# Optimization experiments

Hardware: AMD Instinct MI355X
Metric: run time of the kernel (lower is better)

The kernel has to match this reference:

```python
import math
import jax, jax.numpy as jnp
import numpy as np

B, T, IN_DIM = 8, 2048, 256
HEAD_TOTAL = 256  # out_dim * n_heads
NEG = -1e9


def make_mask(t):
    # torch: tril(ones, diagonal=-1).bool() -> masked_fill(-1e9)
    # i.e., entry (i, j) is -1e9 when j < i (anti-causal), 0 otherwise.
    i = jnp.arange(t)[:, None]
    j = jnp.arange(t)[None, :]
    return jnp.where(j < i, jnp.float32(NEG), jnp.float32(0.0))  # [T, T]


def setup_inputs() -> dict:
    key = jax.random.key(0)
    kx, kq, kk = jax.random.split(key, 3)
    x = jax.random.normal(kx, (B, T, IN_DIM), dtype=jnp.float32)
    # nn.Linear weights are [out_features, in_features]
    s = 1.0 / math.sqrt(IN_DIM)
    Wq = jax.random.uniform(kq, (HEAD_TOTAL, IN_DIM), dtype=jnp.float32, minval=-s, maxval=s)
    Wk = jax.random.uniform(kk, (HEAD_TOTAL, IN_DIM), dtype=jnp.float32, minval=-s, maxval=s)
    return {"x": x, "Wq": Wq, "Wk": Wk}


def reference(x, Wq, Wk):
    # q, k: [B, T, HEAD_TOTAL]
    q = jnp.einsum('bti,oi->bto', x, Wq)
    k = jnp.einsum('bsi,oi->bso', x, Wk)
    scale = 1.0 / math.sqrt(x.shape[-1])  # sqrt(in_dim), as in the source
    mask = make_mask(x.shape[1])
    # e: [B, T, T] masked pre-softmax scores (what the torch forward computes)
    e = jnp.einsum('bto,bso->bts', q, k) * scale + mask
    return e
```

## Files before the change

### kernel.cpp

```cpp
#include <hip/hip_runtime.h>
#include <hip/hip_bf16.h>
#include <stdint.h>

#define B_DIM 8
#define T_DIM 2048
#define INNER 256
#define NEGV (-1e9f)
#define SCALE 0.0625f

typedef __bf16 bf16_t;
typedef __bf16 bf16x8 __attribute__((ext_vector_type(8)));
typedef float f32x4 __attribute__((ext_vector_type(4)));

__device__ inline void gload_lds16(const bf16_t* g, bf16_t* lds) {
  __builtin_amdgcn_global_load_lds(
      (__attribute__((address_space(1))) void*)(g),
      (__attribute__((address_space(3))) void*)(lds),
      16, 0, 0);
}

__device__ inline void stage_tile(const bf16_t* gbase, int ldg,
                                  bf16_t (*lds)[64], int tid) {
  const int l = tid & 63;
  const int w = tid >> 6;
  const int sub = l >> 3;
  const int ce = (l & 7) * 8;
#pragma unroll
  for (int i = 0; i < 4; ++i) {
    const int chunk = i * 4 + w;
    const int row = chunk * 8 + sub;
    gload_lds16(gbase + (size_t)row * ldg + ce, &lds[chunk * 8][0]);
  }
}

__device__ inline void stage_tile_cvt(const float* gbase, int ldg,
                                      bf16_t (*lds)[64], int tid) {
  const int l = tid & 63;
  const int w = tid >> 6;
  const int sub = l >> 3;
  const int ce = (l & 7) * 8;
  f32x4 v[4][2];
#pragma unroll
  for (int i = 0; i < 4; ++i) {
    const int row = (i * 4 + w) * 8 + sub;
    const float* p = gbase + (size_t)row * ldg + ce;
    v[i][0] = *(const f32x4*)p;
    v[i][1] = *(const f32x4*)(p + 4);
  }
#pragma unroll
  for (int i = 0; i < 4; ++i) {
    const int row = (i * 4 + w) * 8 + sub;
    bf16x8 o;
#pragma unroll
    for (int j = 0; j < 4; ++j) {
      o[j]     = (bf16_t)v[i][0][j];
      o[4 + j] = (bf16_t)v[i][1][j];
    }
    *(bf16x8*)&lds[row][ce] = o;
  }
}

template <int KDIM>
__device__ inline void gemm_bt_128(const bf16_t* A, const bf16_t* Bm, int ld,
                                   bf16_t (*Al)[64], bf16_t (*Bl)[64],
                                   f32x4 acc[4][4], int tid) {
  const int l = tid & 63;
  const int wid = tid >> 6;
  const int wr = wid >> 1, wc = wid & 1;
  const int lr = l & 15;
  const int kg = l >> 4;
#pragma unroll
  for (int k0 = 0; k0 < KDIM; k0 += 64) {
    stage_tile(A + k0, ld, Al, tid);
    stage_tile(Bm + k0, ld, Bl, tid);
    __syncthreads();
#pragma unroll
    for (int kk = 0; kk < 2; ++kk) {
      bf16x8 af[4], bfm[4];
#pragma unroll
      for (int f = 0; f < 4; ++f) {
        af[f]  = *(const bf16x8*)&Al[wr * 64 + f * 16 + lr][kk * 32 + kg * 8];
        bfm[f] = *(const bf16x8*)&Bl[wc * 64 + f * 16 + lr][kk * 32 + kg * 8];
      }
#pragma unroll
      for (int m = 0; m < 4; ++m)
#pragma unroll
        for (int n = 0; n < 4; ++n)
          acc[m][n] = __builtin_amdgcn_mfma_f32_16x16x32_bf16(
              af[m], bfm[n], acc[m][n], 0, 0, 0);
    }
    __syncthreads();
  }
}

__global__ __launch_bounds__(256) void proj_kernel(
    const float* __restrict__ x, const float* __restrict__ Wq,
    const float* __restrict__ Wk, bf16_t* __restrict__ Q,
    bf16_t* __restrict__ Kout) {
  __shared__ bf16_t Al[128][64];
  __shared__ bf16_t Bl[128][64];
  const int tid = threadIdx.x;
  const int mrow = blockIdx.x * 128;
  const int ncol = blockIdx.y * 128;
  const float* W = blockIdx.z ? Wk : Wq;
  bf16_t* O = blockIdx.z ? Kout : Q;

  const int l = tid & 63, wid = tid >> 6, wr = wid >> 1, wc = wid & 1;
  const int lr = l & 15, kg = l >> 4;

  f32x4 acc[4][4] = {};
  const float* Ax = x + (size_t)mrow * INNER;
  const float* Bw = W + (size_t)ncol * INNER;
#pragma unroll
  for (int k0 = 0; k0 < INNER; k0 += 64) {
    stage_tile_cvt(Ax + k0, INNER, Al, tid);
    stage_tile_cvt(Bw + k0, INNER, Bl, tid);
    __syncthreads();
#pragma unroll
    for (int kk = 0; kk < 2; ++kk) {
      bf16x8 af[4], bfm[4];
#pragma unroll
      for (int f = 0; f < 4; ++f) {
        af[f]  = *(const bf16x8*)&Al[wr * 64 + f * 16 + lr][kk * 32 + kg * 8];
        bfm[f] = *(const bf16x8*)&Bl[wc * 64 + f * 16 + lr][kk * 32 + kg * 8];
      }
#pragma unroll
      for (int m = 0; m < 4; ++m)
#pragma unroll
        for (int n = 0; n < 4; ++n)
          acc[m][n] = __builtin_amdgcn_mfma_f32_16x16x32_bf16(
              af[m], bfm[n], acc[m][n], 0, 0, 0);
    }
    __syncthreads();
  }

#pragma unroll
  for (int m = 0; m < 4; ++m)
#pragma unroll
    for (int n = 0; n < 4; ++n)
#pragma unroll
      for (int j = 0; j < 4; ++j) {
        int r = mrow + wr * 64 + m * 16 + kg * 4 + j;
        int c = ncol + wc * 64 + n * 16 + lr;
        O[(size_t)r * INNER + c] = (bf16_t)acc[m][n][j];
      }
}

__global__ __launch_bounds__(256) void scores_kernel(
    const bf16_t* __restrict__ Q, const bf16_t* __restrict__ Kin,
    float* __restrict__ E) {
  const int bid = blockIdx.x;
  const int b = bid & 7;
  const int lid = bid >> 3;
  const int rt = lid >> 4;
  const int ct = lid & 15;
  const int tid = threadIdx.x;
  float* Eb = E + (size_t)b * T_DIM * T_DIM;
  const int trow = rt * 128, scol = ct * 128;

  if (ct < rt) {
    const f32x4 neg = {NEGV, NEGV, NEGV, NEGV};
#pragma unroll
    for (int it = 0; it < 16; ++it) {
      int idx = it * 256 + tid;
      int r = idx >> 5, c4 = idx & 31;
      *(f32x4*)&Eb[(size_t)(trow + r) * T_DIM + scol + c4 * 4] = neg;
    }
    return;
  }

  __shared__ bf16_t Al[128][64];
  __shared__ bf16_t Bl[128][64];
  f32x4 acc[4][4] = {};
  const bf16_t* Qb = Q + (size_t)b * T_DIM * INNER;
  const bf16_t* Kb = Kin + (size_t)b * T_DIM * INNER;
  gemm_bt_128<INNER>(Qb + (size_t)trow * INNER, Kb + (size_t)scol * INNER,
                     INNER, Al, Bl, acc, tid);

  const int l = tid & 63, wid = tid >> 6, wr = wid >> 1, wc = wid & 1;
  const int lr = l & 15, kg = l >> 4;
  const bool diag = (ct == rt);
#pragma unroll
  for (int m = 0; m < 4; ++m)
#pragma unroll
    for (int n = 0; n < 4; ++n)
#pragma unroll
      for (int j = 0; j < 4; ++j) {
        int t = trow + wr * 64 + m * 16 + kg * 4 + j;
        int s = scol + wc * 64 + n * 16 + lr;
        float v = acc[m][n][j] * SCALE;
        if (diag && s < t) v += NEGV;
        Eb[(size_t)t * T_DIM + s] = v;
      }
}

extern "C" void kernel_launch(void* const* d_in, const int* in_sizes, int n_in,
                              void* d_out, int out_size, void* d_ws,
                              size_t ws_size, hipStream_t stream) {
  const float* x  = (const float*)d_in[0];
  const float* Wq = (const float*)d_in[1];
  const float* Wk = (const float*)d_in[2];
  float* out = (float*)d_out;

  const size_t n_x = (size_t)B_DIM * T_DIM * INNER;

  bf16_t* Q = (bf16_t*)d_ws;
  bf16_t* K = Q + n_x;

  dim3 g1(B_DIM * T_DIM / 128, INNER / 128, 2);
  proj_kernel<<<g1, dim3(256), 0, stream>>>(x, Wq, Wk, Q, K);

  scores_kernel<<<2048, 256, 0, stream>>>(Q, K, out);
}
```

Before: 47.08 us.

## Widen score tiles to 128x256 with 512-thread blocks

The scores kernel now uses 128x256 output tiles computed by 8 waves instead of 128x128 tiles with 4 waves, halving the block count. Each staged Q tile is reused across twice as many key columns, which cuts redundant global-to-LDS traffic. The fill-only blocks for the fully masked region and the diagonal mask test are adjusted to the wider tiles. The cost is coarser granularity along the diagonal: some tiles that straddle it compute scores that end up masked, and each block uses more LDS.

```diff
diff --git a/kernel.cpp b/kernel.cpp
--- a/kernel.cpp
+++ b/kernel.cpp
@@ -19,15 +19,16 @@
       16, 0, 0);
 }
 
-__device__ inline void stage_tile(const bf16_t* gbase, int ldg,
-                                  bf16_t (*lds)[64], int tid) {
+template <int ROWS>
+__device__ inline void stage_tile512(const bf16_t* gbase, int ldg,
+                                     bf16_t (*lds)[64], int tid) {
   const int l = tid & 63;
   const int w = tid >> 6;
   const int sub = l >> 3;
   const int ce = (l & 7) * 8;
 #pragma unroll
-  for (int i = 0; i < 4; ++i) {
-    const int chunk = i * 4 + w;
+  for (int i = 0; i < ROWS / 64; ++i) {
+    const int chunk = i * 8 + w;
     const int row = chunk * 8 + sub;
     gload_lds16(gbase + (size_t)row * ldg + ce, &lds[chunk * 8][0]);
   }
@@ -57,39 +58,6 @@
       o[4 + j] = (bf16_t)v[i][1][j];
     }
     *(bf16x8*)&lds[row][ce] = o;
-  }
-}
-
-template <int KDIM>
-__device__ inline void gemm_bt_128(const bf16_t* A, const bf16_t* Bm, int ld,
-                                   bf16_t (*Al)[64], bf16_t (*Bl)[64],
-                                   f32x4 acc[4][4], int tid) {
-  const int l = tid & 63;
-  const int wid = tid >> 6;
-  const int wr = wid >> 1, wc = wid & 1;
-  const int lr = l & 15;
-  const int kg = l >> 4;
-#pragma unroll
-  for (int k0 = 0; k0 < KDIM; k0 += 64) {
-    stage_tile(A + k0, ld, Al, tid);
-    stage_tile(Bm + k0, ld, Bl, tid);
-    __syncthreads();
-#pragma unroll
-    for (int kk = 0; kk < 2; ++kk) {
-      bf16x8 af[4], bfm[4];
-#pragma unroll
-      for (int f = 0; f < 4; ++f) {
-        af[f]  = *(const bf16x8*)&Al[wr * 64 + f * 16 + lr][kk * 32 + kg * 8];
-        bfm[f] = *(const bf16x8*)&Bl[wc * 64 + f * 16 + lr][kk * 32 + kg * 8];
-      }
-#pragma unroll
-      for (int m = 0; m < 4; ++m)
-#pragma unroll
-        for (int n = 0; n < 4; ++n)
-          acc[m][n] = __builtin_amdgcn_mfma_f32_16x16x32_bf16(
-              af[m], bfm[n], acc[m][n], 0, 0, 0);
-    }
-    __syncthreads();
   }
 }
 
@@ -146,40 +114,63 @@
       }
 }
 
-__global__ __launch_bounds__(256) void scores_kernel(
+__global__ __launch_bounds__(512) void scores_kernel(
     const bf16_t* __restrict__ Q, const bf16_t* __restrict__ Kin,
     float* __restrict__ E) {
   const int bid = blockIdx.x;
   const int b = bid & 7;
   const int lid = bid >> 3;
-  const int rt = lid >> 4;
-  const int ct = lid & 15;
+  const int rt = lid >> 3;
+  const int ct = lid & 7;
   const int tid = threadIdx.x;
   float* Eb = E + (size_t)b * T_DIM * T_DIM;
-  const int trow = rt * 128, scol = ct * 128;
-
-  if (ct < rt) {
+  const int trow = rt * 128, scol = ct * 256;
+
+  if (scol + 256 <= trow) {
     const f32x4 neg = {NEGV, NEGV, NEGV, NEGV};
 #pragma unroll
     for (int it = 0; it < 16; ++it) {
-      int idx = it * 256 + tid;
-      int r = idx >> 5, c4 = idx & 31;
+      int idx = it * 512 + tid;
+      int r = idx >> 6, c4 = idx & 63;
       *(f32x4*)&Eb[(size_t)(trow + r) * T_DIM + scol + c4 * 4] = neg;
     }
     return;
   }
 
   __shared__ bf16_t Al[128][64];
-  __shared__ bf16_t Bl[128][64];
+  __shared__ bf16_t Bl[256][64];
+  const int l = tid & 63;
+  const int w = tid >> 6;
+  const int wr = w >> 2, wc = w & 3;
+  const int lr = l & 15, kg = l >> 4;
+
   f32x4 acc[4][4] = {};
-  const bf16_t* Qb = Q + (size_t)b * T_DIM * INNER;
-  const bf16_t* Kb = Kin + (size_t)b * T_DIM * INNER;
-  gemm_bt_128<INNER>(Qb + (size_t)trow * INNER, Kb + (size_t)scol * INNER,
-                     INNER, Al, Bl, acc, tid);
-
-  const int l = tid & 63, wid = tid >> 6, wr = wid >> 1, wc = wid & 1;
-  const int lr = l & 15, kg = l >> 4;
-  const bool diag = (ct == rt);
+  const bf16_t* Qb = Q + ((size_t)b * T_DIM + trow) * INNER;
+  const bf16_t* Kb = Kin + ((size_t)b * T_DIM + scol) * INNER;
+#pragma unroll
+  for (int k0 = 0; k0 < INNER; k0 += 64) {
+    stage_tile512<128>(Qb + k0, INNER, Al, tid);
+    stage_tile512<256>(Kb + k0, INNER, Bl, tid);
+    __syncthreads();
+#pragma unroll
+    for (int kk = 0; kk < 2; ++kk) {
+      bf16x8 af[4], bfm[4];
+#pragma unroll
+      for (int f = 0; f < 4; ++f) {
+        af[f]  = *(const bf16x8*)&Al[wr * 64 + f * 16 + lr][kk * 32 + kg * 8];
+        bfm[f] = *(const bf16x8*)&Bl[wc * 64 + f * 16 + lr][kk * 32 + kg * 8];
+      }
+#pragma unroll
+      for (int m = 0; m < 4; ++m)
+#pragma unroll
+        for (int n = 0; n < 4; ++n)
+          acc[m][n] = __builtin_amdgcn_mfma_f32_16x16x32_bf16(
+              af[m], bfm[n], acc[m][n], 0, 0, 0);
+    }
+    __syncthreads();
+  }
+
+  const bool maskable = (scol < trow + 128);
 #pragma unroll
   for (int m = 0; m < 4; ++m)
 #pragma unroll
@@ -189,7 +180,7 @@
         int t = trow + wr * 64 + m * 16 + kg * 4 + j;
         int s = scol + wc * 64 + n * 16 + lr;
         float v = acc[m][n][j] * SCALE;
-        if (diag && s < t) v += NEGV;
+        if (maskable && s < t) v += NEGV;
         Eb[(size_t)t * T_DIM + s] = v;
       }
 }
@@ -210,5 +201,5 @@
   dim3 g1(B_DIM * T_DIM / 128, INNER / 128, 2);
   proj_kernel<<<g1, dim3(256), 0, stream>>>(x, Wq, Wk, Q, K);
 
-  scores_kernel<<<2048, 256, 0, stream>>>(Q, K, out);
-}
+  scores_kernel<<<1024, 512, 0, stream>>>(Q, K, out);
+}
```

Measured after the change: 56.32 us. 19.6% more time.

## Move masked-tile fill into projection kernel to overlap with projection GEMM

Applied to the files above, without the earlier changes.

The -1e9 fill of strictly lower-triangular score tiles moves out of the scores kernel and into the projection kernel. Fill blocks are interleaved with projection compute blocks (odd block ids compute, the rest fill), and a triangular index is recovered with a sqrt formula. The point is to overlap the write-bound fill with the compute-bound projection and to shorten the scores kernel. The costs are a bigger first launch and the reliance on float sqrt to decode the tile index, which the code corrects with a fixup.

```diff
diff --git a/kernel.cpp b/kernel.cpp
--- a/kernel.cpp
+++ b/kernel.cpp
@@ -1,6 +1,7 @@
 #include <hip/hip_runtime.h>
 #include <hip/hip_bf16.h>
 #include <stdint.h>
+#include <math.h>
 
 #define B_DIM 8
 #define T_DIM 2048
@@ -93,18 +94,43 @@
   }
 }
 
-__global__ __launch_bounds__(256) void proj_kernel(
+__global__ __launch_bounds__(256) void proj_fill_kernel(
     const float* __restrict__ x, const float* __restrict__ Wq,
     const float* __restrict__ Wk, bf16_t* __restrict__ Q,
-    bf16_t* __restrict__ Kout) {
+    bf16_t* __restrict__ Kout, float* __restrict__ E) {
+  const int bid = blockIdx.x;
+  const int tid = threadIdx.x;
+
+  const bool is_compute = (bid < 1024) && (bid & 1);
+  if (!is_compute) {
+    int fidx = (bid < 1024) ? (bid >> 1) : (bid - 512);
+    const int b = fidx / 120;
+    int r = fidx - b * 120;
+    int rt = (int)((1.0f + sqrtf(1.0f + 8.0f * (float)r)) * 0.5f);
+    int ct = r - ((rt * (rt - 1)) >> 1);
+    if (ct >= rt) { ct -= rt; rt += 1; }
+    else if (ct < 0) { rt -= 1; ct = r - ((rt * (rt - 1)) >> 1); }
+    float* Eb = E + (size_t)b * T_DIM * T_DIM;
+    const int trow = rt * 128, scol = ct * 128;
+    const f32x4 neg = {NEGV, NEGV, NEGV, NEGV};
+#pragma unroll
+    for (int it = 0; it < 16; ++it) {
+      int idx = it * 256 + tid;
+      int rr = idx >> 5, c4 = idx & 31;
+      *(f32x4*)&Eb[(size_t)(trow + rr) * T_DIM + scol + c4 * 4] = neg;
+    }
+    return;
+  }
+
+  const int idx = bid >> 1;
+  const int mrow = (idx & 127) * 128;
+  const int ncol = ((idx >> 7) & 1) * 128;
+  const int z = idx >> 8;
+  const float* W = z ? Wk : Wq;
+  bf16_t* O = z ? Kout : Q;
+
   __shared__ bf16_t Al[128][64];
   __shared__ bf16_t Bl[128][64];
-  const int tid = threadIdx.x;
-  const int mrow = blockIdx.x * 128;
-  const int ncol = blockIdx.y * 128;
-  const float* W = blockIdx.z ? Wk : Wq;
-  bf16_t* O = blockIdx.z ? Kout : Q;
-
   const int l = tid & 63, wid = tid >> 6, wr = wid >> 1, wc = wid & 1;
   const int lr = l & 15, kg = l >> 4;
 
@@ -140,9 +166,9 @@
     for (int n = 0; n < 4; ++n)
 #pragma unroll
       for (int j = 0; j < 4; ++j) {
-        int r = mrow + wr * 64 + m * 16 + kg * 4 + j;
-        int c = ncol + wc * 64 + n * 16 + lr;
-        O[(size_t)r * INNER + c] = (bf16_t)acc[m][n][j];
+        int rr = mrow + wr * 64 + m * 16 + kg * 4 + j;
+        int cc = ncol + wc * 64 + n * 16 + lr;
+        O[(size_t)rr * INNER + cc] = (bf16_t)acc[m][n][j];
       }
 }
 
@@ -154,20 +180,10 @@
   const int lid = bid >> 3;
   const int rt = lid >> 4;
   const int ct = lid & 15;
+  if (ct < rt) return;
   const int tid = threadIdx.x;
   float* Eb = E + (size_t)b * T_DIM * T_DIM;
   const int trow = rt * 128, scol = ct * 128;
-
-  if (ct < rt) {
-    const f32x4 neg = {NEGV, NEGV, NEGV, NEGV};
-#pragma unroll
-    for (int it = 0; it < 16; ++it) {
-      int idx = it * 256 + tid;
-      int r = idx >> 5, c4 = idx & 31;
-      *(f32x4*)&Eb[(size_t)(trow + r) * T_DIM + scol + c4 * 4] = neg;
-    }
-    return;
-  }
 
   __shared__ bf16_t Al[128][64];
   __shared__ bf16_t Bl[128][64];
@@ -207,8 +223,7 @@
   bf16_t* Q = (bf16_t*)d_ws;
   bf16_t* K = Q + n_x;
 
-  dim3 g1(B_DIM * T_DIM / 128, INNER / 128, 2);
-  proj_kernel<<<g1, dim3(256), 0, stream>>>(x, Wq, Wk, Q, K);
+  proj_fill_kernel<<<1472, 256, 0, stream>>>(x, Wq, Wk, Q, K, out);
 
   scores_kernel<<<2048, 256, 0, stream>>>(Q, K, out);
 }
```

Measured after the change: 53.76 us. 1.14x slower.

## Load MFMA operands directly from global memory in scores kernel, drop LDS staging

Applied to the files above, without the earlier changes.

The scores kernel no longer stages Q and K tiles into shared memory with global_load_lds and barriers. Each lane now reads its bf16x8 MFMA fragments straight from global memory, relying on L1/L2 to serve the overlapping reads across waves. This removes the LDS traffic and __syncthreads, at the cost of duplicated global loads across the 2x2 wave grid and less coalesced access. The kernel is dominated by writing the large output, so the compute-side change may matter little.

```diff
diff --git a/kernel.cpp b/kernel.cpp
--- a/kernel.cpp
+++ b/kernel.cpp
@@ -11,27 +11,6 @@
 typedef __bf16 bf16_t;
 typedef __bf16 bf16x8 __attribute__((ext_vector_type(8)));
 typedef float f32x4 __attribute__((ext_vector_type(4)));
-
-__device__ inline void gload_lds16(const bf16_t* g, bf16_t* lds) {
-  __builtin_amdgcn_global_load_lds(
-      (__attribute__((address_space(1))) void*)(g),
-      (__attribute__((address_space(3))) void*)(lds),
-      16, 0, 0);
-}
-
-__device__ inline void stage_tile(const bf16_t* gbase, int ldg,
-                                  bf16_t (*lds)[64], int tid) {
-  const int l = tid & 63;
-  const int w = tid >> 6;
-  const int sub = l >> 3;
-  const int ce = (l & 7) * 8;
-#pragma unroll
-  for (int i = 0; i < 4; ++i) {
-    const int chunk = i * 4 + w;
-    const int row = chunk * 8 + sub;
-    gload_lds16(gbase + (size_t)row * ldg + ce, &lds[chunk * 8][0]);
-  }
-}
 
 __device__ inline void stage_tile_cvt(const float* gbase, int ldg,
                                       bf16_t (*lds)[64], int tid) {
@@ -57,39 +36,6 @@
       o[4 + j] = (bf16_t)v[i][1][j];
     }
     *(bf16x8*)&lds[row][ce] = o;
-  }
-}
-
-template <int KDIM>
-__device__ inline void gemm_bt_128(const bf16_t* A, const bf16_t* Bm, int ld,
-                                   bf16_t (*Al)[64], bf16_t (*Bl)[64],
-                                   f32x4 acc[4][4], int tid) {
-  const int l = tid & 63;
-  const int wid = tid >> 6;
-  const int wr = wid >> 1, wc = wid & 1;
-  const int lr = l & 15;
-  const int kg = l >> 4;
-#pragma unroll
-  for (int k0 = 0; k0 < KDIM; k0 += 64) {
-    stage_tile(A + k0, ld, Al, tid);
-    stage_tile(Bm + k0, ld, Bl, tid);
-    __syncthreads();
-#pragma unroll
-    for (int kk = 0; kk < 2; ++kk) {
-      bf16x8 af[4], bfm[4];
-#pragma unroll
-      for (int f = 0; f < 4; ++f) {
-        af[f]  = *(const bf16x8*)&Al[wr * 64 + f * 16 + lr][kk * 32 + kg * 8];
-        bfm[f] = *(const bf16x8*)&Bl[wc * 64 + f * 16 + lr][kk * 32 + kg * 8];
-      }
-#pragma unroll
-      for (int m = 0; m < 4; ++m)
-#pragma unroll
-        for (int n = 0; n < 4; ++n)
-          acc[m][n] = __builtin_amdgcn_mfma_f32_16x16x32_bf16(
-              af[m], bfm[n], acc[m][n], 0, 0, 0);
-    }
-    __syncthreads();
   }
 }
 
@@ -169,16 +115,35 @@
     return;
   }
 
-  __shared__ bf16_t Al[128][64];
-  __shared__ bf16_t Bl[128][64];
-  f32x4 acc[4][4] = {};
-  const bf16_t* Qb = Q + (size_t)b * T_DIM * INNER;
-  const bf16_t* Kb = Kin + (size_t)b * T_DIM * INNER;
-  gemm_bt_128<INNER>(Qb + (size_t)trow * INNER, Kb + (size_t)scol * INNER,
-                     INNER, Al, Bl, acc, tid);
-
   const int l = tid & 63, wid = tid >> 6, wr = wid >> 1, wc = wid & 1;
   const int lr = l & 15, kg = l >> 4;
+
+  const bf16_t* qrow[4];
+  const bf16_t* krow[4];
+#pragma unroll
+  for (int f = 0; f < 4; ++f) {
+    qrow[f] = Q + ((size_t)b * T_DIM + trow + wr * 64 + f * 16 + lr) * INNER
+              + kg * 8;
+    krow[f] = Kin + ((size_t)b * T_DIM + scol + wc * 64 + f * 16 + lr) * INNER
+              + kg * 8;
+  }
+
+  f32x4 acc[4][4] = {};
+#pragma unroll
+  for (int kc = 0; kc < 8; ++kc) {
+    bf16x8 af[4], bfm[4];
+#pragma unroll
+    for (int f = 0; f < 4; ++f) af[f]  = *(const bf16x8*)(qrow[f] + kc * 32);
+#pragma unroll
+    for (int f = 0; f < 4; ++f) bfm[f] = *(const bf16x8*)(krow[f] + kc * 32);
+#pragma unroll
+    for (int m = 0; m < 4; ++m)
+#pragma unroll
+      for (int n = 0; n < 4; ++n)
+        acc[m][n] = __builtin_amdgcn_mfma_f32_16x16x32_bf16(
+            af[m], bfm[n], acc[m][n], 0, 0, 0);
+  }
+
   const bool diag = (ct == rt);
 #pragma unroll
   for (int m = 0; m < 4; ++m)
```

Result: slower. 69.97 us (+48.6%).
